# Optimization experiments

Measured on AMD Instinct MI355X. Metric: run time of the kernel, lower is better.

Reference implementation:

```python
import jax, jax.numpy as jnp
import numpy as np

B, S, E, H = 2, 2048, 1024, 16
D = E // H  # head_dim = 64

def setup_inputs() -> dict:
    key = jax.random.key(0)
    ks = jax.random.split(key, 9)
    scale = 1.0 / np.sqrt(E)
    inp = {"x": jax.random.normal(ks[0], (B, S, E), dtype=jnp.float32)}
    for i, name in enumerate(["q", "k", "v", "o"]):
        inp[f"W{name}"] = jax.random.uniform(ks[1 + 2 * i], (E, E), jnp.float32, -scale, scale)
        inp[f"b{name}"] = jax.random.uniform(ks[2 + 2 * i], (E,), jnp.float32, -scale, scale)
    return inp

def reference(x, Wq, bq, Wk, bk, Wv, bv, Wo, bo):
    b, s, e = x.shape
    q = x @ Wq + bq
    k = x @ Wk + bk
    v = x @ Wv + bv
    # Faithful to source: view(B, H, S, D) with NO transpose -> splits the
    # sequence dimension across heads (each head sees a contiguous chunk of
    # s*d elements reinterpreted as [s, d]).
    q = q.reshape(b, H, s, D)
    k = k.reshape(b, H, s, D)
    v = v.reshape(b, H, s, D)
    scores = jnp.einsum("bhqd,bhkd->bhqk", q, k) / np.sqrt(D)
    # mask=False in source still adds a zeros mask (no-op); omitted.
    probs = jax.nn.softmax(scores, axis=-1)
    xhat = jnp.einsum("bhqk,bhkd->bhqd", probs, v)
    # transpose(1, 2).contiguous().view(B, S, E)
    xhat = xhat.transpose(0, 2, 1, 3).reshape(b, s, e)
    return xhat @ Wo + bo
```

## Files before the change

kernel.cpp:

```cpp
#include <hip/hip_runtime.h>
#include <hip/hip_bf16.h>
#include <math.h>

#define B_ 2
#define S_ 2048
#define E_ 1024
#define H_ 16
#define D_ 64

typedef __attribute__((ext_vector_type(8))) short short8;
typedef __attribute__((ext_vector_type(4))) float f32x4;
typedef __attribute__((ext_vector_type(4))) unsigned short us4;
typedef __attribute__((ext_vector_type(8))) unsigned short us8;
typedef unsigned short ushort_t;

#define MFMA16 __builtin_amdgcn_mfma_f32_16x16x32_bf16

__device__ __forceinline__ ushort_t f2bf(float f) {
    unsigned int u = __float_as_uint(f);
    u += 0x7FFFu + ((u >> 16) & 1u);
    return (ushort_t)(u >> 16);
}
__device__ __forceinline__ float bf2f(ushort_t h) {
    return __uint_as_float((unsigned int)h << 16);
}
__device__ __forceinline__ ushort_t f2bf_fast(float f) {
    __hip_bfloat16 h = __float2bfloat16(f);
    return *reinterpret_cast<ushort_t*>(&h);
}

__device__ __forceinline__ void gload16(const void* g, void* l) {
    __builtin_amdgcn_global_load_lds(
        (__attribute__((address_space(1))) void*)(unsigned long long)g,
        (__attribute__((address_space(3))) void*)(unsigned int)(unsigned long long)l,
        16, 0, 0);
}

__global__ __launch_bounds__(256)
void split_x(const float* __restrict__ in, ushort_t* __restrict__ hi)
{
    const size_t base = ((size_t)blockIdx.x * 256 + threadIdx.x) * 8;
    float v[8];
    *reinterpret_cast<float4*>(&v[0]) = *reinterpret_cast<const float4*>(&in[base]);
    *reinterpret_cast<float4*>(&v[4]) = *reinterpret_cast<const float4*>(&in[base + 4]);
    us8 h;
#pragma unroll
    for (int j = 0; j < 8; ++j) h[j] = f2bf(v[j]);
    *reinterpret_cast<us8*>(&hi[base]) = h;
}

__global__ __launch_bounds__(256)
void wsplit_t(const float* __restrict__ Wq, const float* __restrict__ Wk,
              const float* __restrict__ Wv, const float* __restrict__ Wo,
              ushort_t* __restrict__ Wth, ushort_t* __restrict__ Wtl)
{
    __shared__ float T[64][65];
    const int tid = threadIdx.x;
    const int z = blockIdx.z;
    const float* W = (z == 0) ? Wq : (z == 1) ? Wk : (z == 2) ? Wv : Wo;
    const int kt = blockIdx.y * 64;
    const int nt = blockIdx.x * 64;

    const int lr = (tid >> 4) * 4;
    const int lc = (tid & 15) * 4;
#pragma unroll
    for (int i = 0; i < 4; ++i) {
        float4 v = *reinterpret_cast<const float4*>(&W[(size_t)(kt + lr + i) * 1024 + nt + lc]);
        T[lr + i][lc + 0] = v.x; T[lr + i][lc + 1] = v.y;
        T[lr + i][lc + 2] = v.z; T[lr + i][lc + 3] = v.w;
    }
    __syncthreads();

    const int n = tid >> 2;
    const int kc = (tid & 3) * 16;
    us8 h[2], l[2];
#pragma unroll
    for (int u = 0; u < 2; ++u)
#pragma unroll
        for (int j = 0; j < 8; ++j) {
            float v = T[kc + u * 8 + j][n];
            ushort_t hh = f2bf(v);
            h[u][j] = hh;
            l[u][j] = f2bf(v - bf2f(hh));
        }
    ushort_t* dh = Wth + ((size_t)z * 1024 + nt + n) * 1024 + kt + kc;
    ushort_t* dl = Wtl + ((size_t)z * 1024 + nt + n) * 1024 + kt + kc;
    *reinterpret_cast<us8*>(dh)     = h[0];
    *reinterpret_cast<us8*>(dh + 8) = h[1];
    *reinterpret_cast<us8*>(dl)     = l[0];
    *reinterpret_cast<us8*>(dl + 8) = l[1];
}

__global__ __launch_bounds__(256, 3)
void gemm_qkv(const ushort_t* __restrict__ xh, const ushort_t* __restrict__ Wth,
              const float* __restrict__ bq, const float* __restrict__ bk,
              const float* __restrict__ bv,
              ushort_t* __restrict__ Qb, ushort_t* __restrict__ Kb,
              ushort_t* __restrict__ Vb, float qalpha)
{
    __shared__ ushort_t As[128 * 32], Bs[128 * 32];
    const int which = blockIdx.x >> 3;
    const int n0 = (blockIdx.x & 7) * 128;
    const int m0 = blockIdx.y * 128;
    const ushort_t* Bh = Wth + (size_t)which * 1024 * 1024;
    const float* bias = (which == 0) ? bq : (which == 1) ? bk : bv;
    ushort_t* out = (which == 0) ? Qb : (which == 1) ? Kb : Vb;
    const float alpha = (which == 0) ? qalpha : 1.0f;

    const int tid  = threadIdx.x;
    const int lane = tid & 63;
    const int w    = tid >> 6;
    const int l15  = lane & 15;
    const int g    = lane >> 4;
    const int wr   = w >> 1;
    const int wc   = w & 1;

    const int sr  = lane >> 2;
    const int scz = (lane & 3) ^ ((sr >> 1) & 3);
    const int sc  = scz * 8;
    const int j0 = w * 2, j1 = j0 + 1;

    const ushort_t* gA0 = xh + (size_t)(m0 + j0 * 16 + sr) * 1024 + sc;
    const ushort_t* gA1 = xh + (size_t)(m0 + j1 * 16 + sr) * 1024 + sc;
    const ushort_t* gB0 = Bh + (size_t)(n0 + j0 * 16 + sr) * 1024 + sc;
    const ushort_t* gB1 = Bh + (size_t)(n0 + j1 * 16 + sr) * 1024 + sc;

    const int sx  = (l15 >> 1) & 3;
    const int rd1 = (((g >> 1) + 0) ^ sx) * 8 + (g & 1) * 4;
    const int rd2 = (((g >> 1) + 2) ^ sx) * 8 + (g & 1) * 4;

    f32x4 acc[4][4];
#pragma unroll
    for (int i = 0; i < 4; ++i)
#pragma unroll
        for (int j = 0; j < 4; ++j) { acc[i][j][0] = 0.f; acc[i][j][1] = 0.f; acc[i][j][2] = 0.f; acc[i][j][3] = 0.f; }

    for (int kt = 0; kt < 32; ++kt) {
        const int k0 = kt * 32;
        if (kt) __syncthreads();
        gload16(gA0 + k0, As + j0 * 512);
        gload16(gA1 + k0, As + j1 * 512);
        gload16(gB0 + k0, Bs + j0 * 512);
        gload16(gB1 + k0, Bs + j1 * 512);
        asm volatile("s_waitcnt vmcnt(0)" ::: "memory");
        __syncthreads();

        short8 bh[4];
#pragma unroll
        for (int nb = 0; nb < 4; ++nb) {
            const int rb = (wc * 64 + nb * 16 + l15) * 32;
            union { us4 h[2]; short8 s; } u;
            u.h[0] = *reinterpret_cast<const us4*>(Bs + rb + rd1);
            u.h[1] = *reinterpret_cast<const us4*>(Bs + rb + rd2);
            bh[nb] = u.s;
        }
#pragma unroll
        for (int mb = 0; mb < 4; ++mb) {
            const int rb = (wr * 64 + mb * 16 + l15) * 32;
            union { us4 h[2]; short8 s; } ua;
            ua.h[0] = *reinterpret_cast<const us4*>(As + rb + rd1);
            ua.h[1] = *reinterpret_cast<const us4*>(As + rb + rd2);
            const short8 ah = ua.s;
#pragma unroll
            for (int nb = 0; nb < 4; ++nb)
                acc[mb][nb] = MFMA16(ah, bh[nb], acc[mb][nb], 0, 0, 0);
        }
    }

    float bvv[4];
#pragma unroll
    for (int nb = 0; nb < 4; ++nb) bvv[nb] = bias[n0 + wc * 64 + nb * 16 + l15];
#pragma unroll
    for (int mb = 0; mb < 4; ++mb)
#pragma unroll
        for (int r = 0; r < 4; ++r) {
            const size_t row = m0 + wr * 64 + mb * 16 + 4 * g + r;
#pragma unroll
            for (int nb = 0; nb < 4; ++nb) {
                const float vv = (acc[mb][nb][r] + bvv[nb]) * alpha;
                out[row * 1024 + n0 + wc * 64 + nb * 16 + l15] = f2bf(vv);
            }
        }
}

__global__ __launch_bounds__(256, 2)
void gemm_o64(const ushort_t* __restrict__ Ah, const ushort_t* __restrict__ Al,
              const ushort_t* __restrict__ Bh, const ushort_t* __restrict__ Bl,
              const float* __restrict__ bias, float* __restrict__ out)
{
    __shared__ ushort_t AsH[128 * 32], AsL[128 * 32], BsH[64 * 32], BsL[64 * 32];
    const int tid  = threadIdx.x;
    const int lane = tid & 63;
    const int w    = tid >> 6;
    const int l15  = lane & 15;
    const int g    = lane >> 4;
    const int wr   = w >> 1;
    const int wc   = w & 1;
    const int n0 = blockIdx.x * 64;
    const int m0 = blockIdx.y * 128;

    const int sr  = lane >> 2;
    const int scz = (lane & 3) ^ ((sr >> 1) & 3);
    const int sc  = scz * 8;
    const int ja0 = 2 * w, ja1 = 2 * w + 1;

    const ushort_t* gAh0 = Ah + (size_t)(m0 + ja0 * 16 + sr) * 1024 + sc;
    const ushort_t* gAh1 = Ah + (size_t)(m0 + ja1 * 16 + sr) * 1024 + sc;
    const ushort_t* gAl0 = Al + (size_t)(m0 + ja0 * 16 + sr) * 1024 + sc;
    const ushort_t* gAl1 = Al + (size_t)(m0 + ja1 * 16 + sr) * 1024 + sc;
    const ushort_t* gBh0 = Bh + (size_t)(n0 + w * 16 + sr) * 1024 + sc;
    const ushort_t* gBl0 = Bl + (size_t)(n0 + w * 16 + sr) * 1024 + sc;

    const int sx  = (l15 >> 1) & 3;
    const int rd1 = (((g >> 1) + 0) ^ sx) * 8 + (g & 1) * 4;
    const int rd2 = (((g >> 1) + 2) ^ sx) * 8 + (g & 1) * 4;

    f32x4 acc[4][2];
#pragma unroll
    for (int i = 0; i < 4; ++i)
#pragma unroll
        for (int j = 0; j < 2; ++j) { acc[i][j][0] = 0.f; acc[i][j][1] = 0.f; acc[i][j][2] = 0.f; acc[i][j][3] = 0.f; }

    for (int kt = 0; kt < 32; ++kt) {
        const int k0 = kt * 32;
        if (kt) __syncthreads();
        gload16(gAh0 + k0, AsH + ja0 * 512);
        gload16(gAh1 + k0, AsH + ja1 * 512);
        gload16(gAl0 + k0, AsL + ja0 * 512);
        gload16(gAl1 + k0, AsL + ja1 * 512);
        gload16(gBh0 + k0, BsH + w * 512);
        gload16(gBl0 + k0, BsL + w * 512);
        asm volatile("s_waitcnt vmcnt(0)" ::: "memory");
        __syncthreads();

        short8 bh[2], bl[2];
#pragma unroll
        for (int nb = 0; nb < 2; ++nb) {
            const int rb = (wc * 32 + nb * 16 + l15) * 32;
            union { us4 h[2]; short8 s; } u;
            u.h[0] = *reinterpret_cast<const us4*>(BsH + rb + rd1);
            u.h[1] = *reinterpret_cast<const us4*>(BsH + rb + rd2);
            bh[nb] = u.s;
            union { us4 h[2]; short8 s; } v;
            v.h[0] = *reinterpret_cast<const us4*>(BsL + rb + rd1);
            v.h[1] = *reinterpret_cast<const us4*>(BsL + rb + rd2);
            bl[nb] = v.s;
        }
#pragma unroll
        for (int mb = 0; mb < 4; ++mb) {
            const int rb = (wr * 64 + mb * 16 + l15) * 32;
            union { us4 h[2]; short8 s; } ua;
            ua.h[0] = *reinterpret_cast<const us4*>(AsH + rb + rd1);
            ua.h[1] = *reinterpret_cast<const us4*>(AsH + rb + rd2);
            union { us4 h[2]; short8 s; } ul;
            ul.h[0] = *reinterpret_cast<const us4*>(AsL + rb + rd1);
            ul.h[1] = *reinterpret_cast<const us4*>(AsL + rb + rd2);
            const short8 ah = ua.s, al = ul.s;
#pragma unroll
            for (int nb = 0; nb < 2; ++nb) {
                acc[mb][nb] = MFMA16(ah, bh[nb], acc[mb][nb], 0, 0, 0);
                acc[mb][nb] = MFMA16(al, bh[nb], acc[mb][nb], 0, 0, 0);
                acc[mb][nb] = MFMA16(ah, bl[nb], acc[mb][nb], 0, 0, 0);
            }
        }
    }

    float bvv[2];
#pragma unroll
    for (int nb = 0; nb < 2; ++nb) bvv[nb] = bias[n0 + wc * 32 + nb * 16 + l15];
#pragma unroll
    for (int mb = 0; mb < 4; ++mb)
#pragma unroll
        for (int r = 0; r < 4; ++r) {
            const size_t row = m0 + wr * 64 + mb * 16 + 4 * g + r;
#pragma unroll
            for (int nb = 0; nb < 2; ++nb)
                out[row * 1024 + n0 + wc * 32 + nb * 16 + l15] = acc[mb][nb][r] + bvv[nb];
        }
}

__global__ __launch_bounds__(256, 2)
void attn_mfma(const ushort_t* __restrict__ Q, const ushort_t* __restrict__ K,
               const ushort_t* __restrict__ V, ushort_t* __restrict__ XHh,
               ushort_t* __restrict__ XHl)
{
    __shared__ __align__(16) ushort_t Kf[2][4 * 2 * 64 * 8];
    __shared__ __align__(16) ushort_t Vf[2][4 * 2 * 64 * 8];

    const int tid  = threadIdx.x;
    const int w    = tid >> 6;
    const int lane = tid & 63;
    const int l15  = lane & 15;
    const int g    = lane >> 4;

    const int L  = blockIdx.x;
    const int qb = (L >> 3) & 15;
    const int bh = (L & 7) | ((L >> 7) << 3);
    const int b  = bh >> 4;
    const int hh = bh & 15;
    const size_t hoff = (size_t)b * S_ * E_ + (size_t)hh * S_ * D_;
    const ushort_t* Qh = Q + hoff;
    const ushort_t* Kh = K + hoff;
    const ushort_t* Vh = V + hoff;

    const int qw = qb * 128 + w * 32;

    short8 qf[2][2];
#pragma unroll
    for (int qg = 0; qg < 2; ++qg)
#pragma unroll
        for (int m = 0; m < 2; ++m) {
            const ushort_t* src = &Qh[(size_t)(qw + 16 * qg + l15) * D_ + 32 * m + 4 * g];
            us4 lo = *reinterpret_cast<const us4*>(src);
            us4 hi = *reinterpret_cast<const us4*>(src + 16);
            union { us4 h[2]; short8 s; } u;
            u.h[0] = lo; u.h[1] = hi;
            qf[qg][m] = u.s;
        }

    const int kr  = tid >> 2;
    const int kc0 = tid & 3;
    const int kkc = tid >> 4;
    const int vdc = tid & 15;
    const int vmc = kkc >> 3;
    const int vh  = (kkc >> 2) & 1;
    const int vg  = kkc & 3;
    const int vn  = vdc >> 2;

    f32x4 o[2][4];
#pragma unroll
    for (int qg = 0; qg < 2; ++qg)
#pragma unroll
        for (int n = 0; n < 4; ++n)
#pragma unroll
            for (int r = 0; r < 4; ++r) o[qg][n][r] = 0.f;

    float mrun[2] = {-1e30f, -1e30f};
    float lrun[2] = {0.f, 0.f};

    for (int kt = 0; kt < S_ / 128; ++kt) {
        us8 kreg[2][2];
        us4 vreg[2][4];
#pragma unroll
        for (int hf = 0; hf < 2; ++hf) {
            const int rowb = kt * 128 + hf * 64;
#pragma unroll
            for (int u = 0; u < 2; ++u)
                kreg[hf][u] = *reinterpret_cast<const us8*>(&Kh[(size_t)(rowb + kr) * D_ + 8 * (kc0 + 4 * u)]);
#pragma unroll
            for (int i = 0; i < 4; ++i)
                vreg[hf][i] = *reinterpret_cast<const us4*>(&Vh[(size_t)(rowb + 4 * kkc + i) * D_ + 4 * vdc]);
        }

        __syncthreads();

#pragma unroll
        for (int hf = 0; hf < 2; ++hf) {
#pragma unroll
            for (int u = 0; u < 2; ++u) {
                const int c8 = kc0 + 4 * u;
                const int m = c8 >> 2;
                const int h = (c8 >> 1) & 1;
#pragma unroll
                for (int jh = 0; jh < 2; ++jh) {
                    const int gk = (2 * c8 + jh) & 3;
                    const int slot = gk * 16 + (kr & 15);
                    us4 val;
#pragma unroll
                    for (int i = 0; i < 4; ++i) val[i] = (ushort_t)kreg[hf][u][4 * jh + i];
                    *reinterpret_cast<us4*>(&Kf[hf][((((kr >> 4) * 2 + m) * 64 + slot) * 8) + h * 4]) = val;
                }
            }
#pragma unroll
            for (int jj = 0; jj < 4; ++jj) {
                us4 val;
#pragma unroll
                for (int i = 0; i < 4; ++i) val[i] = vreg[hf][i][jj];
                const int pos  = 4 * (vdc & 3) + jj;
                const int posx = pos ^ vg ^ (vn << 2);
                const int slot = vg * 16 + posx;
                *reinterpret_cast<us4*>(&Vf[hf][(((vn * 2 + vmc) * 64 + slot) * 8) + vh * 4]) = val;
            }
        }
        __syncthreads();

        f32x4 s[2][8];
#pragma unroll
        for (int hf = 0; hf < 2; ++hf) {
            short8 kf[4][2];
#pragma unroll
            for (int kkb = 0; kkb < 4; ++kkb)
#pragma unroll
                for (int m = 0; m < 2; ++m)
                    kf[kkb][m] = *reinterpret_cast<const short8*>(&Kf[hf][((kkb * 2 + m) * 64 + lane) * 8]);
#pragma unroll
            for (int qg = 0; qg < 2; ++qg)
#pragma unroll
                for (int kkb = 0; kkb < 4; ++kkb) {
                    f32x4 z; z[0] = 0.f; z[1] = 0.f; z[2] = 0.f; z[3] = 0.f;
                    z = MFMA16(kf[kkb][0], qf[qg][0], z, 0, 0, 0);
                    s[qg][hf * 4 + kkb] = MFMA16(kf[kkb][1], qf[qg][1], z, 0, 0, 0);
                }
        }

#pragma unroll
        for (int qg = 0; qg < 2; ++qg) {
            float t = s[qg][0][0];
#pragma unroll
            for (int j = 0; j < 8; ++j)
#pragma unroll
                for (int r = 0; r < 4; ++r) t = fmaxf(t, s[qg][j][r]);
            t = fmaxf(t, __shfl_xor(t, 16));
            t = fmaxf(t, __shfl_xor(t, 32));
            const float mnew = fmaxf(mrun[qg], t);
            const float corr = __builtin_amdgcn_exp2f(mrun[qg] - mnew);

            float rs = 0.f;
#pragma unroll
            for (int j = 0; j < 8; ++j)
#pragma unroll
                for (int r = 0; r < 4; ++r) {
                    const float p = __builtin_amdgcn_exp2f(s[qg][j][r] - mnew);
                    s[qg][j][r] = p;
                    rs += p;
                }
            rs += __shfl_xor(rs, 16);
            rs += __shfl_xor(rs, 32);
            lrun[qg] = lrun[qg] * corr + rs;
            mrun[qg] = mnew;

#pragma unroll
            for (int r = 0; r < 4; ++r) {
                const float c4 = __shfl(corr, 4 * g + r);
#pragma unroll
                for (int n = 0; n < 4; ++n) o[qg][n][r] *= c4;
            }
        }

#pragma unroll
        for (int hf = 0; hf < 2; ++hf) {
            short8 vf[4][2];
#pragma unroll
            for (int n = 0; n < 4; ++n)
#pragma unroll
                for (int m = 0; m < 2; ++m) {
                    const int posr = (lane & 15) ^ (lane >> 4) ^ (n << 2);
                    const int slot = (lane & 48) | posr;
                    vf[n][m] = *reinterpret_cast<const short8*>(&Vf[hf][((n * 2 + m) * 64 + slot) * 8]);
                }
#pragma unroll
            for (int qg = 0; qg < 2; ++qg) {
                short8 pa[2];
#pragma unroll
                for (int m = 0; m < 2; ++m) {
                    us8 tmp;
#pragma unroll
                    for (int r = 0; r < 4; ++r) {
                        tmp[r]     = f2bf_fast(s[qg][hf * 4 + 2 * m][r]);
                        tmp[r + 4] = f2bf_fast(s[qg][hf * 4 + 2 * m + 1][r]);
                    }
                    union { us8 u8; short8 s8; } cvt; cvt.u8 = tmp;
                    pa[m] = cvt.s8;
                }
#pragma unroll
                for (int n = 0; n < 4; ++n) {
                    o[qg][n] = MFMA16(pa[0], vf[n][0], o[qg][n], 0, 0, 0);
                    o[qg][n] = MFMA16(pa[1], vf[n][1], o[qg][n], 0, 0, 0);
                }
            }
        }
    }

#pragma unroll
    for (int qg = 0; qg < 2; ++qg) {
        const float invl = 1.f / lrun[qg];
#pragma unroll
        for (int r = 0; r < 4; ++r) {
            const float iv = __shfl(invl, 4 * g + r);
            const int row = qw + 16 * qg + 4 * g + r;
            const size_t base = ((size_t)b * S_ + row) * E_ + hh * D_ + l15;
#pragma unroll
            for (int n = 0; n < 4; ++n) {
                const float vv = o[qg][n][r] * iv;
                const ushort_t hi = f2bf(vv);
                XHh[base + 16 * n] = hi;
                XHl[base + 16 * n] = f2bf(vv - bf2f(hi));
            }
        }
    }
}

extern "C" void kernel_launch(void* const* d_in, const int* in_sizes, int n_in,
                              void* d_out, int out_size, void* d_ws, size_t ws_size,
                              hipStream_t stream) {
    (void)in_sizes; (void)n_in; (void)out_size; (void)ws_size;
    const float* x  = (const float*)d_in[0];
    const float* Wq = (const float*)d_in[1];
    const float* bq = (const float*)d_in[2];
    const float* Wk = (const float*)d_in[3];
    const float* bk = (const float*)d_in[4];
    const float* Wv = (const float*)d_in[5];
    const float* bv = (const float*)d_in[6];
    const float* Wo = (const float*)d_in[7];
    const float* bo = (const float*)d_in[8];
    float* out = (float*)d_out;

    char* ws = (char*)d_ws;
    const size_t MB8 = 8ull * 1024 * 1024;
    ushort_t* xhi = (ushort_t*)(ws);
    ushort_t* XHl = (ushort_t*)(ws + MB8);
    ushort_t* Wth = (ushort_t*)(ws + 2 * MB8);
    ushort_t* Wtl = (ushort_t*)(ws + 3 * MB8);
    ushort_t* Qb  = (ushort_t*)(ws + 4 * MB8);
    ushort_t* Kb  = (ushort_t*)(ws + 5 * MB8);
    ushort_t* Vb  = (ushort_t*)(ws + 6 * MB8);
    ushort_t* XHh = xhi;

    const float qalpha = 0.125f * 1.4426950408889634f;

    split_x<<<dim3(2048), dim3(256), 0, stream>>>(x, xhi);
    wsplit_t<<<dim3(16, 16, 4), dim3(256), 0, stream>>>(Wq, Wk, Wv, Wo, Wth, Wtl);

    gemm_qkv<<<dim3(24, 32), dim3(256), 0, stream>>>(xhi, Wth,
                                                     bq, bk, bv, Qb, Kb, Vb, qalpha);

    attn_mfma<<<dim3(512), dim3(256), 0, stream>>>(Qb, Kb, Vb, XHh, XHl);

    gemm_o64<<<dim3(16, 32), dim3(256), 0, stream>>>(XHh, XHl,
                                                     Wth + 3ull * 1024 * 1024,
                                                     Wtl + 3ull * 1024 * 1024,
                                                     bo, out);
}
```

Before: 150.7 us.

## Double-buffer K/V tiles in attention with register prefetch of next tile

Turns the attention kernel's K/V shared-memory staging into a double-buffered pipeline. The next tile's global loads are issued before the current tile's QK MFMAs, and the results are written into the alternate LDS buffer after the softmax. This leaves one barrier per iteration instead of two and hides global load latency behind compute. In exchange LDS use doubles, which may limit occupancy, and kreg/vreg stay live across the loop, raising register pressure.

New measurement: 155.9 us. 3.4% more time.

```diff
diff --git a/kernel.cpp b/kernel.cpp
--- a/kernel.cpp
+++ b/kernel.cpp
@@ -284,8 +284,8 @@
                const ushort_t* __restrict__ V, ushort_t* __restrict__ XHh,
                ushort_t* __restrict__ XHl)
 {
-    __shared__ __align__(16) ushort_t Kf[2][4 * 2 * 64 * 8];
-    __shared__ __align__(16) ushort_t Vf[2][4 * 2 * 64 * 8];
+    __shared__ __align__(16) ushort_t Kf[2][2][4096];
+    __shared__ __align__(16) ushort_t Vf[2][2][4096];
 
     const int tid  = threadIdx.x;
     const int w    = tid >> 6;
@@ -338,51 +338,70 @@
     float mrun[2] = {-1e30f, -1e30f};
     float lrun[2] = {0.f, 0.f};
 
+    us8 kreg[2][2];
+    us4 vreg[2][4];
+
+#define ATTN_LOAD(T)                                                           \
+    {                                                                          \
+        _Pragma("unroll")                                                      \
+        for (int hf = 0; hf < 2; ++hf) {                                       \
+            const int rowb = (T) * 128 + hf * 64;                              \
+            _Pragma("unroll")                                                  \
+            for (int u = 0; u < 2; ++u)                                        \
+                kreg[hf][u] = *reinterpret_cast<const us8*>(                   \
+                    &Kh[(size_t)(rowb + kr) * D_ + 8 * (kc0 + 4 * u)]);        \
+            _Pragma("unroll")                                                  \
+            for (int i = 0; i < 4; ++i)                                        \
+                vreg[hf][i] = *reinterpret_cast<const us4*>(                   \
+                    &Vh[(size_t)(rowb + 4 * kkc + i) * D_ + 4 * vdc]);         \
+        }                                                                      \
+    }
+
+#define ATTN_WRITE(BUF)                                                       \
+    {                                                                          \
+        _Pragma("unroll")                                                      \
+        for (int hf = 0; hf < 2; ++hf) {                                       \
+            _Pragma("unroll")                                                  \
+            for (int u = 0; u < 2; ++u) {                                      \
+                const int c8 = kc0 + 4 * u;                                    \
+                const int mm = c8 >> 2;                                        \
+                const int h8 = (c8 >> 1) & 1;                                  \
+                _Pragma("unroll")                                              \
+                for (int jh = 0; jh < 2; ++jh) {                               \
+                    const int gk = (2 * c8 + jh) & 3;                          \
+                    const int slot = gk * 16 + (kr & 15);                      \
+                    us4 val;                                                   \
+                    _Pragma("unroll")                                          \
+                    for (int i = 0; i < 4; ++i)                                \
+                        val[i] = (ushort_t)kreg[hf][u][4 * jh + i];            \
+                    *reinterpret_cast<us4*>(                                   \
+                        &Kf[BUF][hf][((((kr >> 4) * 2 + mm) * 64 + slot) * 8)  \
+                                     + h8 * 4]) = val;                         \
+                }                                                              \
+            }                                                                  \
+            _Pragma("unroll")                                                  \
+            for (int jj = 0; jj < 4; ++jj) {                                   \
+                us4 val;                                                       \
+                _Pragma("unroll")                                              \
+                for (int i = 0; i < 4; ++i) val[i] = vreg[hf][i][jj];          \
+                const int pos  = 4 * (vdc & 3) + jj;                           \
+                const int posx = pos ^ vg ^ (vn << 2);                         \
+                const int slot = vg * 16 + posx;                               \
+                *reinterpret_cast<us4*>(                                       \
+                    &Vf[BUF][hf][(((vn * 2 + vmc) * 64 + slot) * 8)            \
+                                 + vh * 4]) = val;                             \
+            }                                                                  \
+        }                                                                      \
+    }
+
+    ATTN_LOAD(0);
+    ATTN_WRITE(0);
+    __syncthreads();
+
     for (int kt = 0; kt < S_ / 128; ++kt) {
-        us8 kreg[2][2];
-        us4 vreg[2][4];
-#pragma unroll
-        for (int hf = 0; hf < 2; ++hf) {
-            const int rowb = kt * 128 + hf * 64;
-#pragma unroll
-            for (int u = 0; u < 2; ++u)
-                kreg[hf][u] = *reinterpret_cast<const us8*>(&Kh[(size_t)(rowb + kr) * D_ + 8 * (kc0 + 4 * u)]);
-#pragma unroll
-            for (int i = 0; i < 4; ++i)
-                vreg[hf][i] = *reinterpret_cast<const us4*>(&Vh[(size_t)(rowb + 4 * kkc + i) * D_ + 4 * vdc]);
-        }
-
-        __syncthreads();
-
-#pragma unroll
-        for (int hf = 0; hf < 2; ++hf) {
-#pragma unroll
-            for (int u = 0; u < 2; ++u) {
-                const int c8 = kc0 + 4 * u;
-                const int m = c8 >> 2;
-                const int h = (c8 >> 1) & 1;
-#pragma unroll
-                for (int jh = 0; jh < 2; ++jh) {
-                    const int gk = (2 * c8 + jh) & 3;
-                    const int slot = gk * 16 + (kr & 15);
-                    us4 val;
-#pragma unroll
-                    for (int i = 0; i < 4; ++i) val[i] = (ushort_t)kreg[hf][u][4 * jh + i];
-                    *reinterpret_cast<us4*>(&Kf[hf][((((kr >> 4) * 2 + m) * 64 + slot) * 8) + h * 4]) = val;
-                }
-            }
-#pragma unroll
-            for (int jj = 0; jj < 4; ++jj) {
-                us4 val;
-#pragma unroll
-                for (int i = 0; i < 4; ++i) val[i] = vreg[hf][i][jj];
-                const int pos  = 4 * (vdc & 3) + jj;
-                const int posx = pos ^ vg ^ (vn << 2);
-                const int slot = vg * 16 + posx;
-                *reinterpret_cast<us4*>(&Vf[hf][(((vn * 2 + vmc) * 64 + slot) * 8) + vh * 4]) = val;
-            }
-        }
-        __syncthreads();
+        const int cur = kt & 1;
+
+        if (kt + 1 < S_ / 128) ATTN_LOAD(kt + 1);
 
         f32x4 s[2][8];
 #pragma unroll
@@ -392,7 +411,7 @@
             for (int kkb = 0; kkb < 4; ++kkb)
 #pragma unroll
                 for (int m = 0; m < 2; ++m)
-                    kf[kkb][m] = *reinterpret_cast<const short8*>(&Kf[hf][((kkb * 2 + m) * 64 + lane) * 8]);
+                    kf[kkb][m] = *reinterpret_cast<const short8*>(&Kf[cur][hf][((kkb * 2 + m) * 64 + lane) * 8]);
 #pragma unroll
             for (int qg = 0; qg < 2; ++qg)
 #pragma unroll
@@ -437,6 +456,8 @@
             }
         }
 
+        if (kt + 1 < S_ / 128) ATTN_WRITE(cur ^ 1);
+
 #pragma unroll
         for (int hf = 0; hf < 2; ++hf) {
             short8 vf[4][2];
@@ -446,7 +467,7 @@
                 for (int m = 0; m < 2; ++m) {
                     const int posr = (lane & 15) ^ (lane >> 4) ^ (n << 2);
                     const int slot = (lane & 48) | posr;
-                    vf[n][m] = *reinterpret_cast<const short8*>(&Vf[hf][((n * 2 + m) * 64 + slot) * 8]);
+                    vf[n][m] = *reinterpret_cast<const short8*>(&Vf[cur][hf][((n * 2 + m) * 64 + slot) * 8]);
                 }
 #pragma unroll
             for (int qg = 0; qg < 2; ++qg) {
@@ -469,7 +490,11 @@
                 }
             }
         }
-    }
+
+        __syncthreads();
+    }
+#undef ATTN_LOAD
+#undef ATTN_WRITE
 
 #pragma unroll
     for (int qg = 0; qg < 2; ++qg) {
```

## Double attention block to 512 threads sharing each K/V tile

Applied to the files above, without the earlier changes.

The attention kernel now launches 256 blocks of 512 threads (8 waves) instead of 512 blocks of 256, so each block covers 256 query rows. Each K/V tile staged in shared memory is reused by twice as many waves, and each thread now loads and stages only one 64-row half of the tile instead of both. This halves global K/V traffic per query and the per-thread staging work, but gives fewer blocks and larger 512-thread workgroups, which may reduce scheduling flexibility and occupancy.

After: 147.8 us. About the same (-1.9%).

```diff
diff --git a/kernel.cpp b/kernel.cpp
--- a/kernel.cpp
+++ b/kernel.cpp
@@ -279,13 +279,13 @@
         }
 }
 
-__global__ __launch_bounds__(256, 2)
+__global__ __launch_bounds__(512, 2)
 void attn_mfma(const ushort_t* __restrict__ Q, const ushort_t* __restrict__ K,
                const ushort_t* __restrict__ V, ushort_t* __restrict__ XHh,
                ushort_t* __restrict__ XHl)
 {
-    __shared__ __align__(16) ushort_t Kf[2][4 * 2 * 64 * 8];
-    __shared__ __align__(16) ushort_t Vf[2][4 * 2 * 64 * 8];
+    __shared__ __align__(16) ushort_t Kf[2][4096];
+    __shared__ __align__(16) ushort_t Vf[2][4096];
 
     const int tid  = threadIdx.x;
     const int w    = tid >> 6;
@@ -294,8 +294,8 @@
     const int g    = lane >> 4;
 
     const int L  = blockIdx.x;
-    const int qb = (L >> 3) & 15;
-    const int bh = (L & 7) | ((L >> 7) << 3);
+    const int qb = (L >> 3) & 7;
+    const int bh = (L & 7) | ((L >> 6) << 3);
     const int b  = bh >> 4;
     const int hh = bh & 15;
     const size_t hoff = (size_t)b * S_ * E_ + (size_t)hh * S_ * D_;
@@ -303,7 +303,7 @@
     const ushort_t* Kh = K + hoff;
     const ushort_t* Vh = V + hoff;
 
-    const int qw = qb * 128 + w * 32;
+    const int qw = qb * 256 + w * 32;
 
     short8 qf[2][2];
 #pragma unroll
@@ -318,10 +318,12 @@
             qf[qg][m] = u.s;
         }
 
-    const int kr  = tid >> 2;
-    const int kc0 = tid & 3;
-    const int kkc = tid >> 4;
-    const int vdc = tid & 15;
+    const int hfS  = tid >> 8;
+    const int ltid = tid & 255;
+    const int kr  = ltid >> 2;
+    const int kc0 = ltid & 3;
+    const int kkc = ltid >> 4;
+    const int vdc = ltid & 15;
     const int vmc = kkc >> 3;
     const int vh  = (kkc >> 2) & 1;
     const int vg  = kkc & 3;
@@ -339,48 +341,42 @@
     float lrun[2] = {0.f, 0.f};
 
     for (int kt = 0; kt < S_ / 128; ++kt) {
-        us8 kreg[2][2];
-        us4 vreg[2][4];
-#pragma unroll
-        for (int hf = 0; hf < 2; ++hf) {
-            const int rowb = kt * 128 + hf * 64;
-#pragma unroll
-            for (int u = 0; u < 2; ++u)
-                kreg[hf][u] = *reinterpret_cast<const us8*>(&Kh[(size_t)(rowb + kr) * D_ + 8 * (kc0 + 4 * u)]);
-#pragma unroll
-            for (int i = 0; i < 4; ++i)
-                vreg[hf][i] = *reinterpret_cast<const us4*>(&Vh[(size_t)(rowb + 4 * kkc + i) * D_ + 4 * vdc]);
-        }
+        const int rowb = kt * 128 + hfS * 64;
+        us8 kreg[2];
+#pragma unroll
+        for (int u = 0; u < 2; ++u)
+            kreg[u] = *reinterpret_cast<const us8*>(&Kh[(size_t)(rowb + kr) * D_ + 8 * (kc0 + 4 * u)]);
+        us4 vreg[4];
+#pragma unroll
+        for (int i = 0; i < 4; ++i)
+            vreg[i] = *reinterpret_cast<const us4*>(&Vh[(size_t)(rowb + 4 * kkc + i) * D_ + 4 * vdc]);
 
         __syncthreads();
 
 #pragma unroll
-        for (int hf = 0; hf < 2; ++hf) {
-#pragma unroll
-            for (int u = 0; u < 2; ++u) {
-                const int c8 = kc0 + 4 * u;
-                const int m = c8 >> 2;
-                const int h = (c8 >> 1) & 1;
-#pragma unroll
-                for (int jh = 0; jh < 2; ++jh) {
-                    const int gk = (2 * c8 + jh) & 3;
-                    const int slot = gk * 16 + (kr & 15);
-                    us4 val;
-#pragma unroll
-                    for (int i = 0; i < 4; ++i) val[i] = (ushort_t)kreg[hf][u][4 * jh + i];
-                    *reinterpret_cast<us4*>(&Kf[hf][((((kr >> 4) * 2 + m) * 64 + slot) * 8) + h * 4]) = val;
-                }
+        for (int u = 0; u < 2; ++u) {
+            const int c8 = kc0 + 4 * u;
+            const int m = c8 >> 2;
+            const int h = (c8 >> 1) & 1;
+#pragma unroll
+            for (int jh = 0; jh < 2; ++jh) {
+                const int gk = (2 * c8 + jh) & 3;
+                const int slot = gk * 16 + (kr & 15);
+                us4 val;
+#pragma unroll
+                for (int i = 0; i < 4; ++i) val[i] = (ushort_t)kreg[u][4 * jh + i];
+                *reinterpret_cast<us4*>(&Kf[hfS][((((kr >> 4) * 2 + m) * 64 + slot) * 8) + h * 4]) = val;
             }
-#pragma unroll
-            for (int jj = 0; jj < 4; ++jj) {
-                us4 val;
-#pragma unroll
-                for (int i = 0; i < 4; ++i) val[i] = vreg[hf][i][jj];
-                const int pos  = 4 * (vdc & 3) + jj;
-                const int posx = pos ^ vg ^ (vn << 2);
-                const int slot = vg * 16 + posx;
-                *reinterpret_cast<us4*>(&Vf[hf][(((vn * 2 + vmc) * 64 + slot) * 8) + vh * 4]) = val;
-            }
+        }
+#pragma unroll
+        for (int jj = 0; jj < 4; ++jj) {
+            us4 val;
+#pragma unroll
+            for (int i = 0; i < 4; ++i) val[i] = vreg[i][jj];
+            const int pos  = 4 * (vdc & 3) + jj;
+            const int posx = pos ^ vg ^ (vn << 2);
+            const int slot = vg * 16 + posx;
+            *reinterpret_cast<us4*>(&Vf[hfS][(((vn * 2 + vmc) * 64 + slot) * 8) + vh * 4]) = val;
         }
         __syncthreads();
 
@@ -524,7 +520,7 @@
     gemm_qkv<<<dim3(24, 32), dim3(256), 0, stream>>>(xhi, Wth,
                                                      bq, bk, bv, Qb, Kb, Vb, qalpha);
 
-    attn_mfma<<<dim3(512), dim3(256), 0, stream>>>(Qb, Kb, Vb, XHh, XHl);
+    attn_mfma<<<dim3(256), dim3(512), 0, stream>>>(Qb, Kb, Vb, XHh, XHl);
 
     gemm_o64<<<dim3(16, 32), dim3(256), 0, stream>>>(XHh, XHl,
                                                      Wth + 3ull * 1024 * 1024,
```
